# Performance work log

Hardware: AMD Instinct MI355X
Metric: run time of the kernel (lower is better)

Reference implementation:

```python
import jax, jax.numpy as jnp
import numpy as np

HEAD_NUM = 16


def setup_inputs() -> dict:
    key = jax.random.key(0)
    ks = jax.random.split(key, 7)
    B, S, D = 4, 2048, 1024
    scale = 1.0 / np.sqrt(D)
    return {
        "q": jax.random.normal(ks[0], (B, S, D), jnp.float32),
        "k": jax.random.normal(ks[1], (B, S, D), jnp.float32),
        "v": jax.random.normal(ks[2], (B, S, D), jnp.float32),
        "w_q": jax.random.normal(ks[3], (D, D), jnp.float32) * scale,
        "w_k": jax.random.normal(ks[4], (D, D), jnp.float32) * scale,
        "w_v": jax.random.normal(ks[5], (D, D), jnp.float32) * scale,
        "w_o": jax.random.normal(ks[6], (D, D), jnp.float32) * scale,
    }


def reference(q, k, v, w_q, w_k, w_v, w_o):
    B, Sq, _ = q.shape
    H = HEAD_NUM
    d_k = w_q.shape[1] // H  # per-head key dim

    def split_heads(x):
        b, s, _ = x.shape
        return x.reshape(b, s, H, -1).transpose(0, 2, 1, 3)  # [b,h,s,d]

    hq = split_heads(q @ w_q)
    hk = split_heads(k @ w_k)
    hv = split_heads(v @ w_v)

    scores = jnp.einsum("bhqd,bhkd->bhqk", hq, hk) / jnp.sqrt(
        jnp.asarray(d_k, dtype=hq.dtype)
    )
    attn = jax.nn.softmax(scores, axis=-1)
    out = jnp.einsum("bhqk,bhkd->bhqd", attn, hv)  # [b,h,q,d]
    out = out.transpose(0, 2, 1, 3).reshape(B, Sq, -1)  # concat heads
    return out @ w_o
```

## Files before the change

kernel.cpp:

```cpp
#include <hip/hip_runtime.h>

typedef unsigned short u16;
typedef short vshort8 __attribute__((ext_vector_type(8)));
typedef __bf16 vbf16x8 __attribute__((ext_vector_type(8)));
typedef float vf32x4 __attribute__((ext_vector_type(4)));
typedef float vf32x16 __attribute__((ext_vector_type(16)));

__device__ __forceinline__ u16 f2bf(float f) {
  unsigned u = __builtin_bit_cast(unsigned, f);
  u += 0x7FFFu + ((u >> 16) & 1u);
  return (u16)(u >> 16);
}

__device__ __forceinline__ unsigned cvtpk(float lo, float hi) {
  unsigned r;
  asm("v_cvt_pk_bf16_f32 %0, %1, %2" : "=v"(r) : "v"(lo), "v"(hi));
  return r;
}

__device__ __forceinline__ float swap32f(float x) {
  return __shfl_xor(x, 32);
}

__device__ __forceinline__ vf32x4 mfma_bf16(vshort8 a, vshort8 b, vf32x4 c) {
  return __builtin_amdgcn_mfma_f32_16x16x32_bf16(
      __builtin_bit_cast(vbf16x8, a), __builtin_bit_cast(vbf16x8, b), c, 0, 0, 0);
}

__device__ __forceinline__ vf32x16 mfma32(vshort8 a, vshort8 b, vf32x16 c) {
  return __builtin_amdgcn_mfma_f32_32x32x16_bf16(
      __builtin_bit_cast(vbf16x8, a), __builtin_bit_cast(vbf16x8, b), c, 0, 0, 0);
}

__device__ __forceinline__ void gload16(const void* g, void* l) {
  __builtin_amdgcn_global_load_lds(
      (const __attribute__((address_space(1))) void*)g,
      (__attribute__((address_space(3))) void*)l, 16, 0, 0);
}

__global__ __launch_bounds__(256) void cvtk2(const float* __restrict__ a,
                                             const float* __restrict__ b,
                                             u16* __restrict__ oa,
                                             u16* __restrict__ ob, int n4) {
  const float* in = blockIdx.y ? b : a;
  u16* out = blockIdx.y ? ob : oa;
  if (in == nullptr) return;
  int idx = blockIdx.x * 256 + threadIdx.x;
  int stride = gridDim.x * 256;
  for (int i = idx; i < n4; i += stride) {
    float4 v = ((const float4*)in)[i];
    unsigned lo = (unsigned)f2bf(v.x) | ((unsigned)f2bf(v.y) << 16);
    unsigned hi = (unsigned)f2bf(v.z) | ((unsigned)f2bf(v.w) << 16);
    uint2 o; o.x = lo; o.y = hi;
    *(uint2*)&out[(size_t)i * 4] = o;
  }
}

__global__ __launch_bounds__(256) void wtrans4(const float* __restrict__ w0,
                                               const float* __restrict__ w1,
                                               const float* __restrict__ w2,
                                               const float* __restrict__ w3,
                                               u16* __restrict__ o0, u16* __restrict__ o1,
                                               u16* __restrict__ o2, u16* __restrict__ o3) {
  int z = blockIdx.z;
  const float* W = z == 0 ? w0 : z == 1 ? w1 : z == 2 ? w2 : w3;
  u16* Wt = z == 0 ? o0 : z == 1 ? o1 : z == 2 ? o2 : o3;
  __shared__ u16 tile[64][72];
  int t = threadIdx.x;
  int n0 = blockIdx.x * 64, k0 = blockIdx.y * 64;
#pragma unroll
  for (int it = 0; it < 4; ++it) {
    int cid = it * 256 + t;
    int r = cid >> 4, c4 = cid & 15;
    float4 v = *(const float4*)&W[(k0 + r) * 1024 + n0 + c4 * 4];
    u16* d = &tile[r][c4 * 4];
    d[0] = f2bf(v.x); d[1] = f2bf(v.y); d[2] = f2bf(v.z); d[3] = f2bf(v.w);
  }
  __syncthreads();
#pragma unroll
  for (int it = 0; it < 4; ++it) {
    int cid = it * 256 + t;
    int rn = cid >> 4, c4 = cid & 15;
    unsigned lo = (unsigned)tile[c4 * 4 + 0][rn] | ((unsigned)tile[c4 * 4 + 1][rn] << 16);
    unsigned hi = (unsigned)tile[c4 * 4 + 2][rn] | ((unsigned)tile[c4 * 4 + 3][rn] << 16);
    uint2 o; o.x = lo; o.y = hi;
    *(uint2*)&Wt[(n0 + rn) * 1024 + k0 + c4 * 4] = o;
  }
}

__global__ __launch_bounds__(256) void vtrans(const u16* __restrict__ V,
                                              u16* __restrict__ Vt) {
  __shared__ u16 tile[64][72];
  int t = threadIdx.x;
  int s0 = blockIdx.x * 64;
  int bh = blockIdx.y, b = bh >> 4, h = bh & 15;
#pragma unroll
  for (int it = 0; it < 2; ++it) {
    int cid = it * 256 + t;
    int r = cid >> 3, c8 = cid & 7;
    vshort8 v = *(const vshort8*)&V[(size_t)(b * 2048 + s0 + r) * 1024 + h * 64 + c8 * 8];
    *(vshort8*)&tile[r][c8 * 8] = v;
  }
  __syncthreads();
#pragma unroll
  for (int it = 0; it < 2; ++it) {
    int cid = it * 256 + t;
    int rd = cid >> 3, c8 = cid & 7;
    unsigned w[4];
#pragma unroll
    for (int j = 0; j < 4; ++j) {
      unsigned lo = tile[c8 * 8 + 2 * j][rd];
      unsigned hi = tile[c8 * 8 + 2 * j + 1][rd];
      w[j] = lo | (hi << 16);
    }
    uint4 o; o.x = w[0]; o.y = w[1]; o.z = w[2]; o.w = w[3];
    *(uint4*)&Vt[(size_t)(bh * 64 + rd) * 2048 + s0 + c8 * 8] = o;
  }
}

template <int OUTF32>
__global__ __launch_bounds__(256) void gemm_nt(const u16* __restrict__ A,
                                               const u16* __restrict__ Bt,
                                               float* __restrict__ Cf,
                                               u16* __restrict__ Cb,
                                               int M, int N, int K, float oscale) {
  __shared__ __align__(16) u16 As[128 * 64];
  __shared__ __align__(16) u16 Bs[128 * 64];
  int t = threadIdx.x, lane = t & 63, wid = t >> 6;
  int g = lane >> 4, i16 = lane & 15;
  int n0 = blockIdx.x * 128, m0 = blockIdx.y * 128;
  int wm = wid >> 1, wn = wid & 1;

  vf32x4 acc[4][4];
#pragma unroll
  for (int a = 0; a < 4; ++a)
#pragma unroll
    for (int b = 0; b < 4; ++b) acc[a][b] = (vf32x4){0.f, 0.f, 0.f, 0.f};

  int ldsbase = (wid * 64) * 8;
  for (int kt = 0; kt < K / 64; ++kt) {
    if (kt) __syncthreads();
#pragma unroll
    for (int it = 0; it < 4; ++it) {
      int cid = it * 256 + t;
      int row = cid >> 3, c = cid & 7, sc = c ^ (row & 7);
      gload16(A + (size_t)(m0 + row) * K + kt * 64 + sc * 8, &As[it * 2048 + ldsbase]);
    }
#pragma unroll
    for (int it = 0; it < 4; ++it) {
      int cid = it * 256 + t;
      int row = cid >> 3, c = cid & 7, sc = c ^ (row & 7);
      gload16(Bt + (size_t)(n0 + row) * K + kt * 64 + sc * 8, &Bs[it * 2048 + ldsbase]);
    }
    __syncthreads();
#pragma unroll
    for (int kc = 0; kc < 2; ++kc) {
      vshort8 af[4], bf[4];
#pragma unroll
      for (int mf = 0; mf < 4; ++mf) {
        int row = wm * 64 + mf * 16 + i16;
        int ch = (kc * 4 + g) ^ (row & 7);
        af[mf] = *(const vshort8*)&As[row * 64 + ch * 8];
      }
#pragma unroll
      for (int nf = 0; nf < 4; ++nf) {
        int row = wn * 64 + nf * 16 + i16;
        int ch = (kc * 4 + g) ^ (row & 7);
        bf[nf] = *(const vshort8*)&Bs[row * 64 + ch * 8];
      }
#pragma unroll
      for (int mf = 0; mf < 4; ++mf)
#pragma unroll
        for (int nf = 0; nf < 4; ++nf)
          acc[mf][nf] = mfma_bf16(af[mf], bf[nf], acc[mf][nf]);
    }
  }
#pragma unroll
  for (int mf = 0; mf < 4; ++mf)
#pragma unroll
    for (int nf = 0; nf < 4; ++nf)
#pragma unroll
      for (int r = 0; r < 4; ++r) {
        int m = m0 + wm * 64 + mf * 16 + g * 4 + r;
        int n = n0 + wn * 64 + nf * 16 + i16;
        if (OUTF32)
          Cf[(size_t)m * N + n] = acc[mf][nf][r] * oscale;
        else
          Cb[(size_t)m * N + n] = f2bf(acc[mf][nf][r] * oscale);
      }
}

__device__ __forceinline__ void attn_body(int kt, const u16* __restrict__ Kbase,
                                          const u16* __restrict__ Vbase,
                                          vshort8 (&kfc)[2][4], vshort8 (&kfn)[2][4],
                                          vshort8 (&qf)[2][4], vf32x16 (&oacc)[2][2],
                                          float (&mrun)[2], float (&lrun)[2],
                                          int l31, int hi) {
  int ktn = kt + 1 < 32 ? kt + 1 : 31;
#pragma unroll
  for (int ks = 0; ks < 2; ++ks)
#pragma unroll
    for (int dc = 0; dc < 4; ++dc)
      kfn[ks][dc] = *(const vshort8*)&Kbase[(size_t)(ktn * 64 + ks * 32 + l31) * 1024 + dc * 16 + hi * 8];

  unsigned pk[2][2][8];
#pragma unroll
  for (int fq = 0; fq < 2; ++fq) {
    vf32x16 sacc[2];
#pragma unroll
    for (int ks = 0; ks < 2; ++ks)
#pragma unroll
      for (int r = 0; r < 16; ++r) sacc[ks][r] = 0.f;
    __builtin_amdgcn_s_setprio(1);
#pragma unroll
    for (int dc = 0; dc < 4; ++dc)
#pragma unroll
      for (int ks = 0; ks < 2; ++ks)
        sacc[ks] = mfma32(kfc[ks][dc], qf[fq][dc], sacc[ks]);
    __builtin_amdgcn_s_setprio(0);

    float tm[8];
#pragma unroll
    for (int r = 0; r < 8; ++r)
      tm[r] = fmaxf(fmaxf(sacc[0][r], sacc[0][r + 8]), fmaxf(sacc[1][r], sacc[1][r + 8]));
#pragma unroll
    for (int r = 0; r < 4; ++r) tm[r] = fmaxf(tm[r], tm[r + 4]);
    float pmax = fmaxf(fmaxf(tm[0], tm[1]), fmaxf(tm[2], tm[3]));
    pmax = fmaxf(pmax, swap32f(pmax));

    if (pmax > mrun[fq] + 8.f) {
      float al = exp2f(mrun[fq] - pmax);
      lrun[fq] *= al;
#pragma unroll
      for (int dm = 0; dm < 2; ++dm)
#pragma unroll
        for (int r = 0; r < 16; ++r) oacc[dm][fq][r] *= al;
      mrun[fq] = pmax;
    }
    float mm = mrun[fq];

    float s0 = 0.f, s1 = 0.f, s2 = 0.f, s3 = 0.f;
#pragma unroll
    for (int ks = 0; ks < 2; ++ks)
#pragma unroll
      for (int u = 0; u < 8; ++u) {
        float p0 = exp2f(sacc[ks][2 * u] - mm);
        float p1 = exp2f(sacc[ks][2 * u + 1] - mm);
        pk[fq][ks][u] = cvtpk(p0, p1);
        if (u & 1) { s0 += p0; s1 += p1; } else { s2 += p0; s3 += p1; }
      }
    lrun[fq] += (s0 + s1) + (s2 + s3);
  }

  vshort8 vtf[2][4];
#pragma unroll
  for (int dm = 0; dm < 2; ++dm)
#pragma unroll
    for (int s = 0; s < 4; ++s)
      vtf[dm][s] = *(const vshort8*)&Vbase[(size_t)(dm * 32 + l31) * 2048 + kt * 64 + s * 16 + hi * 8];

#pragma unroll
  for (int s = 0; s < 4; ++s) {
    vshort8 pb[2];
    const int ks = s >> 1, s1b = s & 1;
#pragma unroll
    for (int fq = 0; fq < 2; ++fq) {
      unsigned wA0 = pk[fq][ks][4 * s1b + 0], wA1 = pk[fq][ks][4 * s1b + 1];
      unsigned wB0 = pk[fq][ks][4 * s1b + 2], wB1 = pk[fq][ks][4 * s1b + 3];
      unsigned sA0 = hi ? wB0 : wA0, sA1 = hi ? wB1 : wA1;
      unsigned sd0 = hi ? wA0 : wB0, sd1 = hi ? wA1 : wB1;
      unsigned rv0 = __shfl_xor((int)sd0, 32), rv1 = __shfl_xor((int)sd1, 32);
      uint4 wv;
      wv.x = hi ? rv0 : sA0; wv.y = hi ? rv1 : sA1;
      wv.z = hi ? sA0 : rv0; wv.w = hi ? sA1 : rv1;
      pb[fq] = __builtin_bit_cast(vshort8, wv);
    }
    __builtin_amdgcn_s_setprio(1);
#pragma unroll
    for (int dm = 0; dm < 2; ++dm)
#pragma unroll
      for (int fq = 0; fq < 2; ++fq)
        oacc[dm][fq] = mfma32(vtf[dm][s], pb[fq], oacc[dm][fq]);
    __builtin_amdgcn_s_setprio(0);
  }
}

__global__ __launch_bounds__(512, 2) void attn_fwd4(const u16* __restrict__ Q,
                                                    const u16* __restrict__ K,
                                                    const u16* __restrict__ Vt,
                                                    u16* __restrict__ O) {
  int t = threadIdx.x, lane = t & 63, w = t >> 6;
  int l31 = lane & 31, hi = lane >> 5;
  int i = blockIdx.x;
  int qb = (i >> 3) & 3;
  int bh = (i & 7) + 8 * (i >> 5);
  int b = bh >> 4, h = bh & 15;

  const u16* Qbase = Q + (size_t)(b * 2048 + qb * 512 + w * 64) * 1024 + h * 64;
  const u16* Kbase = K + (size_t)(b * 2048) * 1024 + h * 64;
  const u16* Vbase = Vt + (size_t)(bh * 64) * 2048;

  vshort8 qf[2][4];
#pragma unroll
  for (int fq = 0; fq < 2; ++fq)
#pragma unroll
    for (int dc = 0; dc < 4; ++dc)
      qf[fq][dc] = *(const vshort8*)&Qbase[(size_t)(fq * 32 + l31) * 1024 + dc * 16 + hi * 8];

  vf32x16 oacc[2][2];
#pragma unroll
  for (int dm = 0; dm < 2; ++dm)
#pragma unroll
    for (int fq = 0; fq < 2; ++fq)
#pragma unroll
      for (int r = 0; r < 16; ++r) oacc[dm][fq][r] = 0.f;
  float mrun[2] = {-3.0e38f, -3.0e38f}, lrun[2] = {0.f, 0.f};

  vshort8 kfA[2][4], kfB[2][4];
#pragma unroll
  for (int ks = 0; ks < 2; ++ks)
#pragma unroll
    for (int dc = 0; dc < 4; ++dc)
      kfA[ks][dc] = *(const vshort8*)&Kbase[(size_t)(ks * 32 + l31) * 1024 + dc * 16 + hi * 8];

  for (int kt = 0; kt < 32; kt += 2) {
    attn_body(kt,     Kbase, Vbase, kfA, kfB, qf, oacc, mrun, lrun, l31, hi);
    attn_body(kt + 1, Kbase, Vbase, kfB, kfA, qf, oacc, mrun, lrun, l31, hi);
  }

#pragma unroll
  for (int fq = 0; fq < 2; ++fq) {
    float lt = lrun[fq] + swap32f(lrun[fq]);
    float inv = 1.f / lt;
    size_t qrow = (size_t)(b * 2048 + qb * 512 + w * 64 + fq * 32 + l31);
#pragma unroll
    for (int dm = 0; dm < 2; ++dm)
#pragma unroll
      for (int u = 0; u < 4; ++u) {
        unsigned w0 = cvtpk(oacc[dm][fq][4 * u + 0] * inv, oacc[dm][fq][4 * u + 1] * inv);
        unsigned w1 = cvtpk(oacc[dm][fq][4 * u + 2] * inv, oacc[dm][fq][4 * u + 3] * inv);
        uint2 o; o.x = w0; o.y = w1;
        *(uint2*)&O[qrow * 1024 + h * 64 + dm * 32 + 8 * u + 4 * hi] = o;
      }
  }
}

extern "C" void kernel_launch(void* const* d_in, const int* in_sizes, int n_in,
                              void* d_out, int out_size, void* d_ws, size_t ws_size,
                              hipStream_t stream) {
  const float* q  = (const float*)d_in[0];
  const float* k  = (const float*)d_in[1];
  const float* v  = (const float*)d_in[2];
  const float* wq = (const float*)d_in[3];
  const float* wk = (const float*)d_in[4];
  const float* wv = (const float*)d_in[5];
  const float* wo = (const float*)d_in[6];
  float* out = (float*)d_out;

  const int M = 8192, D = 1024;
  u16* Qb = (u16*)d_out;
  u16* Kb = Qb + (size_t)M * D;
  u16* xb  = (u16*)d_ws;
  u16* Vb  = xb + (size_t)M * D;
  u16* Vtg = Vb + (size_t)M * D;
  u16* wqt = Vtg + (size_t)M * D;
  u16* wkt = wqt + (size_t)D * D;
  u16* wvt = wkt + (size_t)D * D;
  u16* wot = wvt + (size_t)D * D;

  dim3 blk(256);
  wtrans4<<<dim3(16, 16, 4), blk, 0, stream>>>(wq, wk, wv, wo, wqt, wkt, wvt, wot);

  const float QSCALE = 0.125f * 1.44269504088896f;
  int n4 = M * D / 4;
  dim3 ggemm(8, 64);
  cvtk2<<<dim3(1024, 2), blk, 0, stream>>>(q, k, xb, Vtg, n4);
  gemm_nt<0><<<ggemm, blk, 0, stream>>>(xb, wqt, nullptr, Qb, M, D, D, QSCALE);
  gemm_nt<0><<<ggemm, blk, 0, stream>>>(Vtg, wkt, nullptr, Kb, M, D, D, 1.0f);
  cvtk2<<<dim3(1024, 1), blk, 0, stream>>>(v, nullptr, xb, nullptr, n4);
  gemm_nt<0><<<ggemm, blk, 0, stream>>>(xb, wvt, nullptr, Vb, M, D, D, 1.0f);

  vtrans<<<dim3(32, 64), blk, 0, stream>>>(Vb, Vtg);
  attn_fwd4<<<dim3(256), dim3(512), 0, stream>>>(Qb, Kb, Vtg, xb );
  gemm_nt<1><<<ggemm, blk, 0, stream>>>(xb, wot, out, nullptr, M, D, D, 1.0f);
}
```

Before: 265.4 us.

## Split attention KV range across waves and batch Q/K projection GEMMs

The attention kernel now uses 256-thread blocks, each handling 128 queries. Pairs of waves split the key sequence in half, and their softmax state and output accumulators are merged through shared memory, giving 1024 blocks instead of 256. The K register double-buffering is dropped and V fragments are loaded inline. The Q and K projection GEMMs are fused into one launch using blockIdx.z. The aim is more parallelism and occupancy and less launch overhead, at the cost of an LDS merge step, extra shared memory, and a less-hidden K load latency.

```diff
diff --git a/kernel.cpp b/kernel.cpp
--- a/kernel.cpp
+++ b/kernel.cpp
@@ -18,9 +18,7 @@
   return r;
 }
 
-__device__ __forceinline__ float swap32f(float x) {
-  return __shfl_xor(x, 32);
-}
+__device__ __forceinline__ float swap32f(float x) { return __shfl_xor(x, 32); }
 
 __device__ __forceinline__ vf32x4 mfma_bf16(vshort8 a, vshort8 b, vf32x4 c) {
   return __builtin_amdgcn_mfma_f32_16x16x32_bf16(
@@ -119,11 +117,11 @@
 }
 
 template <int OUTF32>
-__global__ __launch_bounds__(256) void gemm_nt(const u16* __restrict__ A,
-                                               const u16* __restrict__ Bt,
-                                               float* __restrict__ Cf,
-                                               u16* __restrict__ Cb,
-                                               int M, int N, int K, float oscale) {
+__device__ __forceinline__ void gemm_core(const u16* __restrict__ A,
+                                          const u16* __restrict__ Bt,
+                                          float* __restrict__ Cf,
+                                          u16* __restrict__ Cb,
+                                          int M, int N, int K, float oscale) {
   __shared__ __align__(16) u16 As[128 * 64];
   __shared__ __align__(16) u16 Bs[128 * 64];
   int t = threadIdx.x, lane = t & 63, wid = t >> 6;
@@ -190,115 +188,46 @@
       }
 }
 
-__device__ __forceinline__ void attn_body(int kt, const u16* __restrict__ Kbase,
-                                          const u16* __restrict__ Vbase,
-                                          vshort8 (&kfc)[2][4], vshort8 (&kfn)[2][4],
-                                          vshort8 (&qf)[2][4], vf32x16 (&oacc)[2][2],
-                                          float (&mrun)[2], float (&lrun)[2],
-                                          int l31, int hi) {
-  int ktn = kt + 1 < 32 ? kt + 1 : 31;
-#pragma unroll
-  for (int ks = 0; ks < 2; ++ks)
-#pragma unroll
-    for (int dc = 0; dc < 4; ++dc)
-      kfn[ks][dc] = *(const vshort8*)&Kbase[(size_t)(ktn * 64 + ks * 32 + l31) * 1024 + dc * 16 + hi * 8];
-
-  unsigned pk[2][2][8];
-#pragma unroll
-  for (int fq = 0; fq < 2; ++fq) {
-    vf32x16 sacc[2];
-#pragma unroll
-    for (int ks = 0; ks < 2; ++ks)
-#pragma unroll
-      for (int r = 0; r < 16; ++r) sacc[ks][r] = 0.f;
-    __builtin_amdgcn_s_setprio(1);
-#pragma unroll
-    for (int dc = 0; dc < 4; ++dc)
-#pragma unroll
-      for (int ks = 0; ks < 2; ++ks)
-        sacc[ks] = mfma32(kfc[ks][dc], qf[fq][dc], sacc[ks]);
-    __builtin_amdgcn_s_setprio(0);
-
-    float tm[8];
-#pragma unroll
-    for (int r = 0; r < 8; ++r)
-      tm[r] = fmaxf(fmaxf(sacc[0][r], sacc[0][r + 8]), fmaxf(sacc[1][r], sacc[1][r + 8]));
-#pragma unroll
-    for (int r = 0; r < 4; ++r) tm[r] = fmaxf(tm[r], tm[r + 4]);
-    float pmax = fmaxf(fmaxf(tm[0], tm[1]), fmaxf(tm[2], tm[3]));
-    pmax = fmaxf(pmax, swap32f(pmax));
-
-    if (pmax > mrun[fq] + 8.f) {
-      float al = exp2f(mrun[fq] - pmax);
-      lrun[fq] *= al;
-#pragma unroll
-      for (int dm = 0; dm < 2; ++dm)
-#pragma unroll
-        for (int r = 0; r < 16; ++r) oacc[dm][fq][r] *= al;
-      mrun[fq] = pmax;
-    }
-    float mm = mrun[fq];
-
-    float s0 = 0.f, s1 = 0.f, s2 = 0.f, s3 = 0.f;
-#pragma unroll
-    for (int ks = 0; ks < 2; ++ks)
-#pragma unroll
-      for (int u = 0; u < 8; ++u) {
-        float p0 = exp2f(sacc[ks][2 * u] - mm);
-        float p1 = exp2f(sacc[ks][2 * u + 1] - mm);
-        pk[fq][ks][u] = cvtpk(p0, p1);
-        if (u & 1) { s0 += p0; s1 += p1; } else { s2 += p0; s3 += p1; }
-      }
-    lrun[fq] += (s0 + s1) + (s2 + s3);
-  }
-
-  vshort8 vtf[2][4];
-#pragma unroll
-  for (int dm = 0; dm < 2; ++dm)
-#pragma unroll
-    for (int s = 0; s < 4; ++s)
-      vtf[dm][s] = *(const vshort8*)&Vbase[(size_t)(dm * 32 + l31) * 2048 + kt * 64 + s * 16 + hi * 8];
-
-#pragma unroll
-  for (int s = 0; s < 4; ++s) {
-    vshort8 pb[2];
-    const int ks = s >> 1, s1b = s & 1;
-#pragma unroll
-    for (int fq = 0; fq < 2; ++fq) {
-      unsigned wA0 = pk[fq][ks][4 * s1b + 0], wA1 = pk[fq][ks][4 * s1b + 1];
-      unsigned wB0 = pk[fq][ks][4 * s1b + 2], wB1 = pk[fq][ks][4 * s1b + 3];
-      unsigned sA0 = hi ? wB0 : wA0, sA1 = hi ? wB1 : wA1;
-      unsigned sd0 = hi ? wA0 : wB0, sd1 = hi ? wA1 : wB1;
-      unsigned rv0 = __shfl_xor((int)sd0, 32), rv1 = __shfl_xor((int)sd1, 32);
-      uint4 wv;
-      wv.x = hi ? rv0 : sA0; wv.y = hi ? rv1 : sA1;
-      wv.z = hi ? sA0 : rv0; wv.w = hi ? sA1 : rv1;
-      pb[fq] = __builtin_bit_cast(vshort8, wv);
-    }
-    __builtin_amdgcn_s_setprio(1);
-#pragma unroll
-    for (int dm = 0; dm < 2; ++dm)
-#pragma unroll
-      for (int fq = 0; fq < 2; ++fq)
-        oacc[dm][fq] = mfma32(vtf[dm][s], pb[fq], oacc[dm][fq]);
-    __builtin_amdgcn_s_setprio(0);
-  }
-}
-
-__global__ __launch_bounds__(512, 2) void attn_fwd4(const u16* __restrict__ Q,
+template <int OUTF32>
+__global__ __launch_bounds__(256) void gemm_nt(const u16* __restrict__ A,
+                                               const u16* __restrict__ Bt,
+                                               float* __restrict__ Cf,
+                                               u16* __restrict__ Cb,
+                                               int M, int N, int K, float oscale) {
+  gemm_core<OUTF32>(A, Bt, Cf, Cb, M, N, K, oscale);
+}
+
+__global__ __launch_bounds__(256) void gemm_nt2(const u16* __restrict__ A0,
+                                                const u16* __restrict__ B0,
+                                                u16* __restrict__ C0, float os0,
+                                                const u16* __restrict__ A1,
+                                                const u16* __restrict__ B1,
+                                                u16* __restrict__ C1, float os1,
+                                                int M, int N, int K) {
+  if (blockIdx.z == 0)
+    gemm_core<0>(A0, B0, nullptr, C0, M, N, K, os0);
+  else
+    gemm_core<0>(A1, B1, nullptr, C1, M, N, K, os1);
+}
+
+__global__ __launch_bounds__(256, 3) void attn_fwd5(const u16* __restrict__ Q,
                                                     const u16* __restrict__ K,
                                                     const u16* __restrict__ Vt,
                                                     u16* __restrict__ O) {
+  __shared__ float2 sm_ml[4][2][64];
+  __shared__ float sm_o[2][64][64];
+
   int t = threadIdx.x, lane = t & 63, w = t >> 6;
   int l31 = lane & 31, hi = lane >> 5;
+  int qg = w >> 1, kh = w & 1;
   int i = blockIdx.x;
-  int qb = (i >> 3) & 3;
-  int bh = (i & 7) + 8 * (i >> 5);
+  int bh = (i & 7) + 8 * (i >> 7);
+  int qc = (i >> 3) & 15;
   int b = bh >> 4, h = bh & 15;
 
-  const u16* Qbase = Q + (size_t)(b * 2048 + qb * 512 + w * 64) * 1024 + h * 64;
-  const u16* Kbase = K + (size_t)(b * 2048) * 1024 + h * 64;
-  const u16* Vbase = Vt + (size_t)(bh * 64) * 2048;
+  const u16* Qbase = Q + (size_t)(b * 2048 + qc * 128 + qg * 64) * 1024 + h * 64;
+  const u16* Kbase = K + (size_t)(b * 2048 + kh * 1024) * 1024 + h * 64;
+  const u16* Vbase = Vt + (size_t)(bh * 64) * 2048 + kh * 1024;
 
   vshort8 qf[2][4];
 #pragma unroll
@@ -316,32 +245,128 @@
       for (int r = 0; r < 16; ++r) oacc[dm][fq][r] = 0.f;
   float mrun[2] = {-3.0e38f, -3.0e38f}, lrun[2] = {0.f, 0.f};
 
-  vshort8 kfA[2][4], kfB[2][4];
-#pragma unroll
-  for (int ks = 0; ks < 2; ++ks)
-#pragma unroll
-    for (int dc = 0; dc < 4; ++dc)
-      kfA[ks][dc] = *(const vshort8*)&Kbase[(size_t)(ks * 32 + l31) * 1024 + dc * 16 + hi * 8];
-
-  for (int kt = 0; kt < 32; kt += 2) {
-    attn_body(kt,     Kbase, Vbase, kfA, kfB, qf, oacc, mrun, lrun, l31, hi);
-    attn_body(kt + 1, Kbase, Vbase, kfB, kfA, qf, oacc, mrun, lrun, l31, hi);
-  }
-
+  for (int kt = 0; kt < 16; ++kt) {
+    vshort8 kf[2][4];
+#pragma unroll
+    for (int ks = 0; ks < 2; ++ks)
+#pragma unroll
+      for (int dc = 0; dc < 4; ++dc)
+        kf[ks][dc] = *(const vshort8*)&Kbase[(size_t)(kt * 64 + ks * 32 + l31) * 1024 + dc * 16 + hi * 8];
+
+#pragma unroll
+    for (int fq = 0; fq < 2; ++fq) {
+      vf32x16 sacc[2];
+#pragma unroll
+      for (int ks = 0; ks < 2; ++ks)
+#pragma unroll
+        for (int r = 0; r < 16; ++r) sacc[ks][r] = 0.f;
+      __builtin_amdgcn_s_setprio(1);
+#pragma unroll
+      for (int dc = 0; dc < 4; ++dc)
+#pragma unroll
+        for (int ks = 0; ks < 2; ++ks)
+          sacc[ks] = mfma32(kf[ks][dc], qf[fq][dc], sacc[ks]);
+      __builtin_amdgcn_s_setprio(0);
+
+      float tm[8];
+#pragma unroll
+      for (int r = 0; r < 8; ++r)
+        tm[r] = fmaxf(fmaxf(sacc[0][r], sacc[0][r + 8]), fmaxf(sacc[1][r], sacc[1][r + 8]));
+#pragma unroll
+      for (int r = 0; r < 4; ++r) tm[r] = fmaxf(tm[r], tm[r + 4]);
+      float pmax = fmaxf(fmaxf(tm[0], tm[1]), fmaxf(tm[2], tm[3]));
+      pmax = fmaxf(pmax, swap32f(pmax));
+
+      if (pmax > mrun[fq] + 8.f) {
+        float al = exp2f(mrun[fq] - pmax);
+        lrun[fq] *= al;
+#pragma unroll
+        for (int dm = 0; dm < 2; ++dm)
+#pragma unroll
+          for (int r = 0; r < 16; ++r) oacc[dm][fq][r] *= al;
+        mrun[fq] = pmax;
+      }
+      float mm = mrun[fq];
+
+#pragma unroll
+      for (int ks = 0; ks < 2; ++ks) {
+        unsigned pkb[8];
+        float s0 = 0.f, s1 = 0.f, s2 = 0.f, s3 = 0.f;
+#pragma unroll
+        for (int u = 0; u < 8; ++u) {
+          float p0 = exp2f(sacc[ks][2 * u] - mm);
+          float p1 = exp2f(sacc[ks][2 * u + 1] - mm);
+          pkb[u] = cvtpk(p0, p1);
+          if (u & 1) { s0 += p0; s1 += p1; } else { s2 += p0; s3 += p1; }
+        }
+        lrun[fq] += (s0 + s1) + (s2 + s3);
+
+#pragma unroll
+        for (int sl = 0; sl < 2; ++sl) {
+          unsigned wA0 = pkb[4 * sl + 0], wA1 = pkb[4 * sl + 1];
+          unsigned wB0 = pkb[4 * sl + 2], wB1 = pkb[4 * sl + 3];
+          unsigned sA0 = hi ? wB0 : wA0, sA1 = hi ? wB1 : wA1;
+          unsigned sd0 = hi ? wA0 : wB0, sd1 = hi ? wA1 : wB1;
+          unsigned rv0 = __shfl_xor((int)sd0, 32), rv1 = __shfl_xor((int)sd1, 32);
+          uint4 wv;
+          wv.x = hi ? rv0 : sA0; wv.y = hi ? rv1 : sA1;
+          wv.z = hi ? sA0 : rv0; wv.w = hi ? sA1 : rv1;
+          vshort8 pb = __builtin_bit_cast(vshort8, wv);
+          __builtin_amdgcn_s_setprio(1);
+#pragma unroll
+          for (int dm = 0; dm < 2; ++dm) {
+            vshort8 vt = *(const vshort8*)&Vbase[(size_t)(dm * 32 + l31) * 2048 +
+                                                 kt * 64 + (2 * ks + sl) * 16 + hi * 8];
+            oacc[dm][fq] = mfma32(vt, pb, oacc[dm][fq]);
+          }
+          __builtin_amdgcn_s_setprio(0);
+        }
+      }
+    }
+  }
+
+  sm_ml[w][0][lane] = make_float2(mrun[0], lrun[0]);
+  sm_ml[w][1][lane] = make_float2(mrun[1], lrun[1]);
+  __syncthreads();
+  float fs[2], flt[2];
 #pragma unroll
   for (int fq = 0; fq < 2; ++fq) {
-    float lt = lrun[fq] + swap32f(lrun[fq]);
-    float inv = 1.f / lt;
-    size_t qrow = (size_t)(b * 2048 + qb * 512 + w * 64 + fq * 32 + l31);
+    float2 p = sm_ml[w ^ 1][fq][lane];
+    float ms = fmaxf(mrun[fq], p.x);
+    fs[fq] = exp2f(mrun[fq] - ms);
+    float fp = exp2f(p.x - ms);
+    flt[fq] = lrun[fq] * fs[fq] + p.y * fp;
+  }
+  if (kh == 1) {
 #pragma unroll
     for (int dm = 0; dm < 2; ++dm)
 #pragma unroll
-      for (int u = 0; u < 4; ++u) {
-        unsigned w0 = cvtpk(oacc[dm][fq][4 * u + 0] * inv, oacc[dm][fq][4 * u + 1] * inv);
-        unsigned w1 = cvtpk(oacc[dm][fq][4 * u + 2] * inv, oacc[dm][fq][4 * u + 3] * inv);
-        uint2 o; o.x = w0; o.y = w1;
-        *(uint2*)&O[qrow * 1024 + h * 64 + dm * 32 + 8 * u + 4 * hi] = o;
-      }
+      for (int fq = 0; fq < 2; ++fq)
+#pragma unroll
+        for (int r = 0; r < 16; ++r)
+          sm_o[qg][dm * 32 + fq * 16 + r][lane] = oacc[dm][fq][r] * fs[fq];
+  }
+  __syncthreads();
+  if (kh == 0) {
+#pragma unroll
+    for (int fq = 0; fq < 2; ++fq) {
+      float lt = flt[fq] + swap32f(flt[fq]);
+      float inv = 1.f / lt;
+      size_t qrow = (size_t)(b * 2048 + qc * 128 + qg * 64 + fq * 32 + l31);
+#pragma unroll
+      for (int dm = 0; dm < 2; ++dm)
+#pragma unroll
+        for (int u = 0; u < 4; ++u) {
+          float c0 = oacc[dm][fq][4 * u + 0] * fs[fq] + sm_o[qg][dm * 32 + fq * 16 + 4 * u + 0][lane];
+          float c1 = oacc[dm][fq][4 * u + 1] * fs[fq] + sm_o[qg][dm * 32 + fq * 16 + 4 * u + 1][lane];
+          float c2 = oacc[dm][fq][4 * u + 2] * fs[fq] + sm_o[qg][dm * 32 + fq * 16 + 4 * u + 2][lane];
+          float c3 = oacc[dm][fq][4 * u + 3] * fs[fq] + sm_o[qg][dm * 32 + fq * 16 + 4 * u + 3][lane];
+          unsigned w0 = cvtpk(c0 * inv, c1 * inv);
+          unsigned w1 = cvtpk(c2 * inv, c3 * inv);
+          uint2 o; o.x = w0; o.y = w1;
+          *(uint2*)&O[qrow * 1024 + h * 64 + dm * 32 + 8 * u + 4 * hi] = o;
+        }
+    }
   }
 }
 
@@ -373,14 +398,13 @@
 
   const float QSCALE = 0.125f * 1.44269504088896f;
   int n4 = M * D / 4;
-  dim3 ggemm(8, 64);
   cvtk2<<<dim3(1024, 2), blk, 0, stream>>>(q, k, xb, Vtg, n4);
-  gemm_nt<0><<<ggemm, blk, 0, stream>>>(xb, wqt, nullptr, Qb, M, D, D, QSCALE);
-  gemm_nt<0><<<ggemm, blk, 0, stream>>>(Vtg, wkt, nullptr, Kb, M, D, D, 1.0f);
+  gemm_nt2<<<dim3(8, 64, 2), blk, 0, stream>>>(xb, wqt, Qb, QSCALE,
+                                               Vtg, wkt, Kb, 1.0f, M, D, D);
   cvtk2<<<dim3(1024, 1), blk, 0, stream>>>(v, nullptr, xb, nullptr, n4);
-  gemm_nt<0><<<ggemm, blk, 0, stream>>>(xb, wvt, nullptr, Vb, M, D, D, 1.0f);
+  gemm_nt<0><<<dim3(8, 64), blk, 0, stream>>>(xb, wvt, nullptr, Vb, M, D, D, 1.0f);
 
   vtrans<<<dim3(32, 64), blk, 0, stream>>>(Vb, Vtg);
-  attn_fwd4<<<dim3(256), dim3(512), 0, stream>>>(Qb, Kb, Vtg, xb );
-  gemm_nt<1><<<ggemm, blk, 0, stream>>>(xb, wot, out, nullptr, M, D, D, 1.0f);
-}
+  attn_fwd5<<<dim3(1024), blk, 0, stream>>>(Qb, Kb, Vtg, xb );
+  gemm_nt<1><<<dim3(8, 64), blk, 0, stream>>>(xb, wot, out, nullptr, M, D, D, 1.0f);
+}
```

Measured after the change: 455.6 us. +71.7%, slower.
